# Kernel optimization log

Measured on AMD Instinct MI355X. Metric: run time of the kernel, lower is better.

## Reference

```python
import jax, jax.numpy as jnp
import numpy as np

N = 100000
E = 1600000
D = 64
N_LAYERS = 2


def setup_inputs() -> dict:
    key = jax.random.key(0)
    ks = jax.random.split(key, 4 + 4 * N_LAYERS)
    h = jax.random.normal(ks[0], (N, D), dtype=jnp.float32)
    x = jax.random.normal(ks[1], (N, 3), dtype=jnp.float32)
    edge_index = jax.random.randint(ks[2], (2, E), 0, N, dtype=jnp.int64)
    node_mask = jnp.ones((N, 1), dtype=jnp.float32)
    scale = 1.0 / np.sqrt(D)
    params = {}
    for i in range(N_LAYERS):
        params[f'W1_{i}'] = jax.random.normal(ks[4 + 4 * i], (D, D), dtype=jnp.float32) * scale
        params[f'b1_{i}'] = jax.random.normal(ks[5 + 4 * i], (D,), dtype=jnp.float32) * scale
        params[f'W2_{i}'] = jax.random.normal(ks[6 + 4 * i], (D, D), dtype=jnp.float32) * scale
        params[f'b2_{i}'] = jax.random.normal(ks[7 + 4 * i], (D,), dtype=jnp.float32) * scale
    return dict(h=h, x=x, edge_index=edge_index, node_mask=node_mask, **params)


def _gin_layer(h, src, dst, W1, b1, W2, b2):
    # GINConv with eps=0: mlp(h_i + sum_{j->i} h_j)
    agg = jax.ops.segment_sum(h[src], dst, num_segments=N)  # [N, D]
    z = h + agg
    z = jax.nn.relu(z @ W1 + b1)
    return z @ W2 + b2


def reference(h, x, edge_index, node_mask,
              W1_0, b1_0, W2_0, b2_0,
              W1_1, b1_1, W2_1, b2_1):
    src, dst = edge_index[0], edge_index[1]
    h = _gin_layer(h, src, dst, W1_0, b1_0, W2_0, b2_0)
    h = _gin_layer(h, src, dst, W1_1, b1_1, W2_1, b2_1)
    h = h * node_mask
    return (h, x)
```

## Files before the change

### kernel.cpp

```cpp
#include <hip/hip_runtime.h>


#define NN 100000
#define EE 1600000
#define CAP 48
#define NBIN 1024
#define CHB 6250
#define OVF_CAPN 8000

#define OVFC_OFF   1024
#define OVF_OFF    1026
#define BSTART_OFF 17056
#define CURSOR_OFF 18112
#define CNT_OFF    19200
#define BUCK_OFF   119296
#define BINNED_OFF 4919296
#define HB_OFF     4919296
#define PW_OFF     8119296

typedef __attribute__((ext_vector_type(8))) short s8v;
typedef __attribute__((ext_vector_type(4))) float f4v;

union U8 { unsigned u[4]; s8v s; };

static __device__ __forceinline__ unsigned short f2bf(float f) {
  unsigned u = __float_as_uint(f);
  return (unsigned short)((u + 0x7FFF + ((u >> 16) & 1)) >> 16);
}
static __device__ __forceinline__ float bf2f(unsigned short s) {
  return __uint_as_float(((unsigned)s) << 16);
}
static __device__ __forceinline__ unsigned pk2(float lo, float hi) {
  return (unsigned)f2bf(lo) | ((unsigned)f2bf(hi) << 16);
}

__global__ __launch_bounds__(256) void hist_k(const int* __restrict__ dst,
                                              int* __restrict__ binTot) {
  __shared__ int hist[NBIN];
  const int t = threadIdx.x;
#pragma unroll
  for (int b = t; b < NBIN; b += 256) hist[b] = 0;
  __syncthreads();
  const int s = blockIdx.x * CHB;
#pragma unroll 1
  for (int i = s + t; i < s + CHB; i += 256) atomicAdd(&hist[dst[i] >> 7], 1);
  __syncthreads();
#pragma unroll
  for (int b = t; b < NBIN; b += 256) {
    const int c = hist[b];
    if (c) atomicAdd(&binTot[b], c);
  }
}

__global__ __launch_bounds__(1024) void scan_k(const int* __restrict__ binTot,
                                               int* __restrict__ binStart,
                                               int* __restrict__ cursor) {
  __shared__ int sh[NBIN];
  const int t = threadIdx.x;
  const int v = binTot[t];
  sh[t] = v;
  __syncthreads();
  for (int off = 1; off < NBIN; off <<= 1) {
    const int x = (t >= off) ? sh[t - off] : 0;
    __syncthreads();
    sh[t] += x;
    __syncthreads();
  }
  binStart[t] = sh[t] - v;
  cursor[t] = sh[t] - v;
  if (t == NBIN - 1) binStart[NBIN] = sh[t];
}

__global__ __launch_bounds__(256) void scatter_k(const int* __restrict__ src,
                                                 const int* __restrict__ dst,
                                                 int* __restrict__ cursor,
                                                 int* __restrict__ binned) {
  __shared__ int hist[NBIN], base[NBIN], lcnt[NBIN];
  const int t = threadIdx.x;
#pragma unroll
  for (int b = t; b < NBIN; b += 256) { hist[b] = 0; lcnt[b] = 0; }
  __syncthreads();
  const int s = blockIdx.x * CHB;
#pragma unroll 1
  for (int i = s + t; i < s + CHB; i += 256) atomicAdd(&hist[dst[i] >> 7], 1);
  __syncthreads();
#pragma unroll
  for (int b = t; b < NBIN; b += 256) {
    const int c = hist[b];
    base[b] = c ? atomicAdd(&cursor[b], c) : 0;
  }
  __syncthreads();
#pragma unroll 1
  for (int i = s + t; i < s + CHB; i += 256) {
    const int d = dst[i], sv = src[i];
    const int bin = d >> 7;
    const int off = atomicAdd(&lcnt[bin], 1);
    binned[base[bin] + off] = ((d & 127) << 17) | sv;
  }
}

__global__ __launch_bounds__(256) void bucketize_k(const int* __restrict__ binStart,
                                                   const int* __restrict__ binned,
                                                   int* __restrict__ bucket,
                                                   int* __restrict__ cnt,
                                                   int* __restrict__ ovf) {
  __shared__ int c128[128];
  const int t = threadIdx.x;
  const int bin = blockIdx.x;
  const int nbase = bin << 7;
  if (t < 128) c128[t] = 0;
  __syncthreads();
  const int s0 = binStart[bin], s1 = binStart[bin + 1];
#pragma unroll 1
  for (int i = s0 + t; i < s1; i += 256) {
    const int p = binned[i];
    const int dlow = p >> 17;
    const int sv = p & 131071;
    const int slot = atomicAdd(&c128[dlow], 1);
    if (slot < CAP) {
      bucket[(nbase + dlow) * CAP + slot] = sv;
    } else {
      const int q = atomicAdd(&ovf[-2], 1);
      if (q < OVF_CAPN) { ovf[2 * q] = nbase + dlow; ovf[2 * q + 1] = sv; }
    }
  }
  __syncthreads();
  if (t < 128 && nbase + t < NN) cnt[nbase + t] = c128[t];
}

__global__ __launch_bounds__(256) void cvt_k(const float* __restrict__ h,
                                             unsigned* __restrict__ hb) {
  const int i = blockIdx.x * blockDim.x + threadIdx.x;
  if (i >= NN * 8) return;
  const float4* __restrict__ h4 = reinterpret_cast<const float4*>(h);
  const float4 a = h4[2 * i], b = h4[2 * i + 1];
  uint4 o;
  o.x = pk2(a.x, a.y); o.y = pk2(a.z, a.w);
  o.z = pk2(b.x, b.y); o.w = pk2(b.z, b.w);
  reinterpret_cast<uint4*>(hb)[i] = o;
}

__global__ __launch_bounds__(256) void pack_k(const float* __restrict__ W1a,
                                              const float* __restrict__ W2a,
                                              const float* __restrict__ W1b,
                                              const float* __restrict__ W2b,
                                              unsigned short* __restrict__ pw) {
  const int t = threadIdx.x;
  const float* Ws[4] = {W1a, W2a, W1b, W2b};
#pragma unroll
  for (int m = 0; m < 4; ++m) {
    const float* __restrict__ W = Ws[m];
#pragma unroll 1
    for (int i = 0; i < 16; ++i) {
      const int e = i * 256 + t;
      const int j = e & 7;
      const int lv = (e >> 3) & 63;
      const int ks = (e >> 9) & 1;
      const int tt = e >> 10;
      const int k = ks * 32 + (lv >> 4) * 8 + j;
      const int n = tt * 16 + (lv & 15);
      pw[m * 4096 + e] = f2bf(W[k * 64 + n]);
    }
  }
}

__global__ __launch_bounds__(256) void agg_k(const unsigned short* __restrict__ hb,
                                             const int* __restrict__ cnt,
                                             const int* __restrict__ bucket,
                                             char* __restrict__ zb) {
  const int l = threadIdx.x & 63;
  int n = blockIdx.x * (blockDim.x >> 6) + (threadIdx.x >> 6);
  if (n >= NN) return;
  n = __builtin_amdgcn_readfirstlane(n);
  const int deg = min(cnt[n], CAP);
  const int* __restrict__ brow = bucket + n * CAP;
  float acc = bf2f(hb[(n << 6) | l]);
#pragma unroll 1
  for (int e = 0; e < deg; e += 8) {
    const int4 qa = *reinterpret_cast<const int4*>(brow + e);
    const int4 qb = *reinterpret_cast<const int4*>(brow + e + 4);
    const int s0 = qa.x;
    const int s1 = (e + 1 < deg) ? qa.y : s0;
    const int s2 = (e + 2 < deg) ? qa.z : s0;
    const int s3 = (e + 3 < deg) ? qa.w : s0;
    const int s4 = (e + 4 < deg) ? qb.x : s0;
    const int s5 = (e + 5 < deg) ? qb.y : s0;
    const int s6 = (e + 6 < deg) ? qb.z : s0;
    const int s7 = (e + 7 < deg) ? qb.w : s0;
    const float v0 = bf2f(hb[(s0 << 6) | l]);
    const float v1 = bf2f(hb[(s1 << 6) | l]);
    const float v2 = bf2f(hb[(s2 << 6) | l]);
    const float v3 = bf2f(hb[(s3 << 6) | l]);
    const float v4 = bf2f(hb[(s4 << 6) | l]);
    const float v5 = bf2f(hb[(s5 << 6) | l]);
    const float v6 = bf2f(hb[(s6 << 6) | l]);
    const float v7 = bf2f(hb[(s7 << 6) | l]);
    const float w1 = (e + 1 < deg) ? v1 : 0.f;
    const float w2 = (e + 2 < deg) ? v2 : 0.f;
    const float w3 = (e + 3 < deg) ? v3 : 0.f;
    const float w4 = (e + 4 < deg) ? v4 : 0.f;
    const float w5 = (e + 5 < deg) ? v5 : 0.f;
    const float w6 = (e + 6 < deg) ? v6 : 0.f;
    const float w7 = (e + 7 < deg) ? v7 : 0.f;
    acc += ((v0 + w1) + (w2 + w3)) + ((w4 + w5) + (w6 + w7));
  }
  *reinterpret_cast<unsigned short*>(zb + n * 256 + l * 2) = f2bf(acc);
}

__global__ __launch_bounds__(256) void ovf_fix_k(const unsigned short* __restrict__ hb,
                                                 char* __restrict__ zb,
                                                 const int* __restrict__ ovfCnt,
                                                 const int* __restrict__ ovf) {
  const int cv = min(ovfCnt[0], OVF_CAPN);
  const int l = threadIdx.x & 63;
  const int w = threadIdx.x >> 6;
  for (int p = w; p < cv; p += 4) {
    const int d = ovf[2 * p];
    const int s = ovf[2 * p + 1];
    const float add = bf2f(hb[(s << 6) | l]);
    unsigned* wp = reinterpret_cast<unsigned*>(zb + d * 256 + (l >> 1) * 4);
    const bool hi = l & 1;
    unsigned cur = atomicAdd(wp, 0u);
    while (true) {
      const unsigned short hv = hi ? (unsigned short)(cur >> 16) : (unsigned short)(cur & 0xffffu);
      const unsigned short nh = f2bf(bf2f(hv) + add);
      const unsigned nw = hi ? ((cur & 0x0000ffffu) | ((unsigned)nh << 16))
                             : ((cur & 0xffff0000u) | (unsigned)nh);
      const unsigned prev = atomicCAS(wp, cur, nw);
      if (prev == cur) break;
      cur = prev;
    }
  }
}

template <int OUTBF>
__global__ __launch_bounds__(256) void mlp_mfma_k(
    const char* __restrict__ zb,
    void* __restrict__ hout,
    const unsigned short* __restrict__ pw1, const float* __restrict__ b1,
    const unsigned short* __restrict__ pw2, const float* __restrict__ b2,
    const float* __restrict__ mask) {
  __shared__ unsigned ldsu[128 * 33];
  const int tid = threadIdx.x;
  const int w = tid >> 6, l = tid & 63, g = l >> 4, mi = l & 15;
  const int m0 = blockIdx.x * 128;
  const int rbase = w * 32;

  s8v zf[2][2];
#pragma unroll
  for (int tm = 0; tm < 2; ++tm) {
    const int node = m0 + rbase + tm * 16 + mi;
    const int nc = node < NN ? node : NN - 1;
#pragma unroll
    for (int ks = 0; ks < 2; ++ks)
      zf[tm][ks] = *reinterpret_cast<const s8v*>(zb + nc * 256 + (ks * 32 + g * 8) * 2);
  }

  f4v acc[4][2];
#pragma unroll
  for (int t = 0; t < 4; ++t) {
    const f4v bv = *reinterpret_cast<const f4v*>(b1 + t * 16 + g * 4);
    acc[t][0] = bv; acc[t][1] = bv;
  }
#pragma unroll
  for (int t = 0; t < 4; ++t) {
#pragma unroll
    for (int ks = 0; ks < 2; ++ks) {
      const s8v wf = *reinterpret_cast<const s8v*>(pw1 + ((t * 2 + ks) * 64 + l) * 8);
#pragma unroll
      for (int tm = 0; tm < 2; ++tm)
        acc[t][tm] = __builtin_amdgcn_mfma_f32_16x16x32_bf16(wf, zf[tm][ks], acc[t][tm], 0, 0, 0);
    }
  }

#pragma unroll
  for (int t = 0; t < 4; ++t) {
#pragma unroll
    for (int tm = 0; tm < 2; ++tm) {
      const f4v a = acc[t][tm];
      const int row = rbase + tm * 16 + mi;
      const int base = row * 33 + t * 8 + g * 2;
      ldsu[base]     = pk2(fmaxf(a.x, 0.f), fmaxf(a.y, 0.f));
      ldsu[base + 1] = pk2(fmaxf(a.z, 0.f), fmaxf(a.w, 0.f));
    }
  }
  __syncthreads();

  s8v cf[2][2];
#pragma unroll
  for (int tm = 0; tm < 2; ++tm) {
    const int row = rbase + tm * 16 + mi;
    const int cbase = row * 33 + (mi < 0 ? 0 : 0);
#pragma unroll
    for (int ks = 0; ks < 2; ++ks) {
      const int b0 = row * 33 + ks * 16 + g * 4;
      U8 u8;
      u8.u[0] = ldsu[b0 + 0];
      u8.u[1] = ldsu[b0 + 1];
      u8.u[2] = ldsu[b0 + 2];
      u8.u[3] = ldsu[b0 + 3];
      cf[tm][ks] = u8.s;
    }
    (void)cbase;
  }

  f4v acc2[4][2];
#pragma unroll
  for (int t = 0; t < 4; ++t) {
    const f4v bv = *reinterpret_cast<const f4v*>(b2 + t * 16 + g * 4);
    acc2[t][0] = bv; acc2[t][1] = bv;
  }
#pragma unroll
  for (int t = 0; t < 4; ++t) {
#pragma unroll
    for (int ks = 0; ks < 2; ++ks) {
      const s8v wf = *reinterpret_cast<const s8v*>(pw2 + ((t * 2 + ks) * 64 + l) * 8);
#pragma unroll
      for (int tm = 0; tm < 2; ++tm)
        acc2[t][tm] = __builtin_amdgcn_mfma_f32_16x16x32_bf16(wf, cf[tm][ks], acc2[t][tm], 0, 0, 0);
    }
  }

  if (OUTBF) {
    unsigned* __restrict__ ho = reinterpret_cast<unsigned*>(hout);
#pragma unroll
    for (int tm = 0; tm < 2; ++tm) {
      const int node = m0 + rbase + tm * 16 + mi;
      if (node < NN) {
#pragma unroll
        for (int t = 0; t < 4; ++t) {
          const f4v a = acc2[t][tm];
          const int idx = node * 32 + t * 8 + g * 2;
          uint2 p;
          p.x = pk2(a.x, a.y);
          p.y = pk2(a.z, a.w);
          *reinterpret_cast<uint2*>(&ho[idx]) = p;
        }
      }
    }
  } else {
    float* __restrict__ fo = reinterpret_cast<float*>(hout);
#pragma unroll
    for (int tm = 0; tm < 2; ++tm) {
      const int node = m0 + rbase + tm * 16 + mi;
      if (node < NN) {
        const float mv = mask[node];
#pragma unroll
        for (int t = 0; t < 4; ++t) {
          f4v v = acc2[t][tm];
          v *= mv;
          *reinterpret_cast<f4v*>(fo + node * 64 + t * 16 + g * 4) = v;
        }
      }
    }
  }
}

__global__ __launch_bounds__(256) void xcopy_k(const float* __restrict__ x,
                                               float* __restrict__ ox) {
  const int i = blockIdx.x * blockDim.x + threadIdx.x;
  if (i < (NN * 3) / 4) {
    reinterpret_cast<float4*>(ox)[i] = reinterpret_cast<const float4*>(x)[i];
  }
}

extern "C" void kernel_launch(void* const* d_in, const int* in_sizes, int n_in,
                              void* d_out, int out_size, void* d_ws, size_t ws_size,
                              hipStream_t stream) {
  (void)in_sizes; (void)n_in; (void)out_size; (void)ws_size;
  const float* h    = (const float*)d_in[0];
  const float* x    = (const float*)d_in[1];
  const int*   ei   = (const int*)d_in[2];
  const float* mask = (const float*)d_in[3];
  const float* W1_0 = (const float*)d_in[4];
  const float* b1_0 = (const float*)d_in[5];
  const float* W2_0 = (const float*)d_in[6];
  const float* b2_0 = (const float*)d_in[7];
  const float* W1_1 = (const float*)d_in[8];
  const float* b1_1 = (const float*)d_in[9];
  const float* W2_1 = (const float*)d_in[10];
  const float* b2_1 = (const float*)d_in[11];
  float* out = (float*)d_out;

  const int* src = ei;
  const int* dst = ei + EE;

  int* wsp       = (int*)d_ws;
  int* binTot    = wsp;
  int* ovfCnt    = wsp + OVFC_OFF;
  int* ovf       = wsp + OVF_OFF;
  int* binStart  = wsp + BSTART_OFF;
  int* cursor    = wsp + CURSOR_OFF;
  int* cnt       = wsp + CNT_OFF;
  int* bucket    = wsp + BUCK_OFF;
  int* binned    = wsp + BINNED_OFF;
  unsigned* hb   = (unsigned*)(wsp + HB_OFF);
  unsigned short* pw = (unsigned short*)(wsp + PW_OFF);
  const unsigned short* hbs = (const unsigned short*)hb;
  char* zb       = (char*)d_out;

  hipMemsetAsync(d_ws, 0, 8192, stream);
  hist_k<<<256, 256, 0, stream>>>(dst, binTot);
  scan_k<<<1, 1024, 0, stream>>>(binTot, binStart, cursor);
  scatter_k<<<256, 256, 0, stream>>>(src, dst, cursor, binned);
  bucketize_k<<<782, 256, 0, stream>>>(binStart, binned, bucket, cnt, ovf);

  pack_k<<<1, 256, 0, stream>>>(W1_0, W2_0, W1_1, W2_1, pw);

  cvt_k<<<3125, 256, 0, stream>>>(h, hb);
  agg_k<<<25000, 256, 0, stream>>>(hbs, cnt, bucket, zb);
  ovf_fix_k<<<1, 256, 0, stream>>>(hbs, zb, ovfCnt, ovf);
  mlp_mfma_k<1><<<782, 256, 0, stream>>>(zb, hb, pw, b1_0, pw + 4096, b2_0, nullptr);

  agg_k<<<25000, 256, 0, stream>>>(hbs, cnt, bucket, zb);
  ovf_fix_k<<<1, 256, 0, stream>>>(hbs, zb, ovfCnt, ovf);
  mlp_mfma_k<0><<<782, 256, 0, stream>>>(zb, out, pw + 8192, b1_1, pw + 12288, b2_1, mask);

  xcopy_k<<<293, 256, 0, stream>>>(x, out + NN * 64);
}
```

Before: 178.1 us.

## Restructure aggregation to 4 neighbor groups per wave and merge small launches

The aggregation kernel now splits each wave into four 16-lane groups. Each lane loads four bf16 features (8 bytes) per neighbor, the groups process up to 32 neighbors per iteration, and partial sums are reduced with cross-lane shuffles. This exposes more independent gathers per wave and uses wider loads, at the cost of shuffle work and wasted lanes on low-degree nodes. The memset and weight packing are fused into one setup kernel, the x copy is merged into the bf16 conversion kernel, and the histogram and scatter loops read edges as int2 pairs to cut launch overhead and load instructions.

```diff
diff --git a/kernel.cpp b/kernel.cpp
--- a/kernel.cpp
+++ b/kernel.cpp
@@ -34,6 +34,33 @@
   return (unsigned)f2bf(lo) | ((unsigned)f2bf(hi) << 16);
 }
 
+__global__ __launch_bounds__(256) void setup_k(const float* __restrict__ W1a,
+                                               const float* __restrict__ W2a,
+                                               const float* __restrict__ W1b,
+                                               const float* __restrict__ W2b,
+                                               unsigned short* __restrict__ pw,
+                                               int* __restrict__ wsp) {
+  const int t = threadIdx.x;
+#pragma unroll
+  for (int i = t; i < 2048; i += 256) wsp[i] = 0;
+  const float* Ws[4] = {W1a, W2a, W1b, W2b};
+#pragma unroll
+  for (int m = 0; m < 4; ++m) {
+    const float* __restrict__ W = Ws[m];
+#pragma unroll 1
+    for (int i = 0; i < 16; ++i) {
+      const int e = i * 256 + t;
+      const int j = e & 7;
+      const int lv = (e >> 3) & 63;
+      const int ks = (e >> 9) & 1;
+      const int tt = e >> 10;
+      const int k = ks * 32 + (lv >> 4) * 8 + j;
+      const int n = tt * 16 + (lv & 15);
+      pw[m * 4096 + e] = f2bf(W[k * 64 + n]);
+    }
+  }
+}
+
 __global__ __launch_bounds__(256) void hist_k(const int* __restrict__ dst,
                                               int* __restrict__ binTot) {
   __shared__ int hist[NBIN];
@@ -43,7 +70,11 @@
   __syncthreads();
   const int s = blockIdx.x * CHB;
 #pragma unroll 1
-  for (int i = s + t; i < s + CHB; i += 256) atomicAdd(&hist[dst[i] >> 7], 1);
+  for (int p = t; p < CHB / 2; p += 256) {
+    const int2 dd = *reinterpret_cast<const int2*>(dst + s + 2 * p);
+    atomicAdd(&hist[dd.x >> 7], 1);
+    atomicAdd(&hist[dd.y >> 7], 1);
+  }
   __syncthreads();
 #pragma unroll
   for (int b = t; b < NBIN; b += 256) {
@@ -82,7 +113,11 @@
   __syncthreads();
   const int s = blockIdx.x * CHB;
 #pragma unroll 1
-  for (int i = s + t; i < s + CHB; i += 256) atomicAdd(&hist[dst[i] >> 7], 1);
+  for (int p = t; p < CHB / 2; p += 256) {
+    const int2 dd = *reinterpret_cast<const int2*>(dst + s + 2 * p);
+    atomicAdd(&hist[dd.x >> 7], 1);
+    atomicAdd(&hist[dd.y >> 7], 1);
+  }
   __syncthreads();
 #pragma unroll
   for (int b = t; b < NBIN; b += 256) {
@@ -91,11 +126,16 @@
   }
   __syncthreads();
 #pragma unroll 1
-  for (int i = s + t; i < s + CHB; i += 256) {
-    const int d = dst[i], sv = src[i];
-    const int bin = d >> 7;
-    const int off = atomicAdd(&lcnt[bin], 1);
-    binned[base[bin] + off] = ((d & 127) << 17) | sv;
+  for (int p = t; p < CHB / 2; p += 256) {
+    const int i = s + 2 * p;
+    const int2 dd = *reinterpret_cast<const int2*>(dst + i);
+    const int2 ss = *reinterpret_cast<const int2*>(src + i);
+    int bin = dd.x >> 7;
+    int off = atomicAdd(&lcnt[bin], 1);
+    binned[base[bin] + off] = ((dd.x & 127) << 17) | ss.x;
+    bin = dd.y >> 7;
+    off = atomicAdd(&lcnt[bin], 1);
+    binned[base[bin] + off] = ((dd.y & 127) << 17) | ss.y;
   }
 }
 
@@ -128,83 +168,87 @@
   if (t < 128 && nbase + t < NN) cnt[nbase + t] = c128[t];
 }
 
-__global__ __launch_bounds__(256) void cvt_k(const float* __restrict__ h,
-                                             unsigned* __restrict__ hb) {
-  const int i = blockIdx.x * blockDim.x + threadIdx.x;
-  if (i >= NN * 8) return;
-  const float4* __restrict__ h4 = reinterpret_cast<const float4*>(h);
-  const float4 a = h4[2 * i], b = h4[2 * i + 1];
-  uint4 o;
-  o.x = pk2(a.x, a.y); o.y = pk2(a.z, a.w);
-  o.z = pk2(b.x, b.y); o.w = pk2(b.z, b.w);
-  reinterpret_cast<uint4*>(hb)[i] = o;
-}
-
-__global__ __launch_bounds__(256) void pack_k(const float* __restrict__ W1a,
-                                              const float* __restrict__ W2a,
-                                              const float* __restrict__ W1b,
-                                              const float* __restrict__ W2b,
-                                              unsigned short* __restrict__ pw) {
-  const int t = threadIdx.x;
-  const float* Ws[4] = {W1a, W2a, W1b, W2b};
-#pragma unroll
-  for (int m = 0; m < 4; ++m) {
-    const float* __restrict__ W = Ws[m];
-#pragma unroll 1
-    for (int i = 0; i < 16; ++i) {
-      const int e = i * 256 + t;
-      const int j = e & 7;
-      const int lv = (e >> 3) & 63;
-      const int ks = (e >> 9) & 1;
-      const int tt = e >> 10;
-      const int k = ks * 32 + (lv >> 4) * 8 + j;
-      const int n = tt * 16 + (lv & 15);
-      pw[m * 4096 + e] = f2bf(W[k * 64 + n]);
-    }
+__global__ __launch_bounds__(256) void cvtx_k(const float* __restrict__ h,
+                                              unsigned* __restrict__ hb,
+                                              const float* __restrict__ x,
+                                              float* __restrict__ ox) {
+  const int b = blockIdx.x;
+  const int t = threadIdx.x;
+  if (b < 3125) {
+    const int i = b * 256 + t;
+    const float4* __restrict__ h4 = reinterpret_cast<const float4*>(h);
+    const float4 a = h4[2 * i], c = h4[2 * i + 1];
+    uint4 o;
+    o.x = pk2(a.x, a.y); o.y = pk2(a.z, a.w);
+    o.z = pk2(c.x, c.y); o.w = pk2(c.z, c.w);
+    reinterpret_cast<uint4*>(hb)[i] = o;
+  } else {
+    const int i = (b - 3125) * 256 + t;
+    if (i < (NN * 3) / 4)
+      reinterpret_cast<float4*>(ox)[i] = reinterpret_cast<const float4*>(x)[i];
   }
 }
 
 __global__ __launch_bounds__(256) void agg_k(const unsigned short* __restrict__ hb,
                                              const int* __restrict__ cnt,
                                              const int* __restrict__ bucket,
-                                             char* __restrict__ zb) {
+                                             unsigned* __restrict__ zbu) {
   const int l = threadIdx.x & 63;
-  int n = blockIdx.x * (blockDim.x >> 6) + (threadIdx.x >> 6);
+  const int s = l >> 4, g = l & 15;
+  int n = blockIdx.x * 4 + (threadIdx.x >> 6);
+  n = __builtin_amdgcn_readfirstlane(n);
   if (n >= NN) return;
-  n = __builtin_amdgcn_readfirstlane(n);
   const int deg = min(cnt[n], CAP);
   const int* __restrict__ brow = bucket + n * CAP;
-  float acc = bf2f(hb[(n << 6) | l]);
-#pragma unroll 1
-  for (int e = 0; e < deg; e += 8) {
-    const int4 qa = *reinterpret_cast<const int4*>(brow + e);
-    const int4 qb = *reinterpret_cast<const int4*>(brow + e + 4);
-    const int s0 = qa.x;
-    const int s1 = (e + 1 < deg) ? qa.y : s0;
-    const int s2 = (e + 2 < deg) ? qa.z : s0;
-    const int s3 = (e + 3 < deg) ? qa.w : s0;
-    const int s4 = (e + 4 < deg) ? qb.x : s0;
-    const int s5 = (e + 5 < deg) ? qb.y : s0;
-    const int s6 = (e + 6 < deg) ? qb.z : s0;
-    const int s7 = (e + 7 < deg) ? qb.w : s0;
-    const float v0 = bf2f(hb[(s0 << 6) | l]);
-    const float v1 = bf2f(hb[(s1 << 6) | l]);
-    const float v2 = bf2f(hb[(s2 << 6) | l]);
-    const float v3 = bf2f(hb[(s3 << 6) | l]);
-    const float v4 = bf2f(hb[(s4 << 6) | l]);
-    const float v5 = bf2f(hb[(s5 << 6) | l]);
-    const float v6 = bf2f(hb[(s6 << 6) | l]);
-    const float v7 = bf2f(hb[(s7 << 6) | l]);
-    const float w1 = (e + 1 < deg) ? v1 : 0.f;
-    const float w2 = (e + 2 < deg) ? v2 : 0.f;
-    const float w3 = (e + 3 < deg) ? v3 : 0.f;
-    const float w4 = (e + 4 < deg) ? v4 : 0.f;
-    const float w5 = (e + 5 < deg) ? v5 : 0.f;
-    const float w6 = (e + 6 < deg) ? v6 : 0.f;
-    const float w7 = (e + 7 < deg) ? v7 : 0.f;
-    acc += ((v0 + w1) + (w2 + w3)) + ((w4 + w5) + (w6 + w7));
-  }
-  *reinterpret_cast<unsigned short*>(zb + n * 256 + l * 2) = f2bf(acc);
+  const uint2* __restrict__ h2 = reinterpret_cast<const uint2*>(hb);
+
+  const uint2 sv = h2[n * 16 + g];
+  const unsigned m0 = (s == 0) ? sv.x : 0u;
+  const unsigned m1 = (s == 0) ? sv.y : 0u;
+  float a0 = __uint_as_float(m0 << 16);
+  float a1 = __uint_as_float(m0 & 0xffff0000u);
+  float a2 = __uint_as_float(m1 << 16);
+  float a3 = __uint_as_float(m1 & 0xffff0000u);
+
+#pragma unroll 1
+  for (int it = 0; it * 32 < deg; ++it) {
+    const int base = it * 32 + s * 8;
+    const int4 qa = *reinterpret_cast<const int4*>(brow + base);
+    const int4 qb = *reinterpret_cast<const int4*>(brow + base + 4);
+    const bool k0 = base + 0 < deg, k1 = base + 1 < deg, k2 = base + 2 < deg, k3 = base + 3 < deg;
+    const bool k4 = base + 4 < deg, k5 = base + 5 < deg, k6 = base + 6 < deg, k7 = base + 7 < deg;
+    const int i0 = k0 ? qa.x : n, i1 = k1 ? qa.y : n, i2 = k2 ? qa.z : n, i3 = k3 ? qa.w : n;
+    const int i4 = k4 ? qb.x : n, i5 = k5 ? qb.y : n, i6 = k6 ? qb.z : n, i7 = k7 ? qb.w : n;
+    const uint2 v0 = h2[i0 * 16 + g];
+    const uint2 v1 = h2[i1 * 16 + g];
+    const uint2 v2 = h2[i2 * 16 + g];
+    const uint2 v3 = h2[i3 * 16 + g];
+    const uint2 v4 = h2[i4 * 16 + g];
+    const uint2 v5 = h2[i5 * 16 + g];
+    const uint2 v6 = h2[i6 * 16 + g];
+    const uint2 v7 = h2[i7 * 16 + g];
+#define ACC(vv, kk)                                                      \
+    { const unsigned ux = kk ? vv.x : 0u, uy = kk ? vv.y : 0u;           \
+      a0 += __uint_as_float(ux << 16);                                   \
+      a1 += __uint_as_float(ux & 0xffff0000u);                           \
+      a2 += __uint_as_float(uy << 16);                                   \
+      a3 += __uint_as_float(uy & 0xffff0000u); }
+    ACC(v0, k0) ACC(v1, k1) ACC(v2, k2) ACC(v3, k3)
+    ACC(v4, k4) ACC(v5, k5) ACC(v6, k6) ACC(v7, k7)
+#undef ACC
+  }
+
+  a0 += __shfl_xor(a0, 16); a1 += __shfl_xor(a1, 16);
+  a2 += __shfl_xor(a2, 16); a3 += __shfl_xor(a3, 16);
+  a0 += __shfl_xor(a0, 32); a1 += __shfl_xor(a1, 32);
+  a2 += __shfl_xor(a2, 32); a3 += __shfl_xor(a3, 32);
+
+  if (s == 0) {
+    uint2 o;
+    o.x = pk2(a0, a1);
+    o.y = pk2(a2, a3);
+    reinterpret_cast<uint2*>(zbu)[n * 32 + g] = o;
+  }
 }
 
 __global__ __launch_bounds__(256) void ovf_fix_k(const unsigned short* __restrict__ hb,
@@ -290,7 +334,6 @@
 #pragma unroll
   for (int tm = 0; tm < 2; ++tm) {
     const int row = rbase + tm * 16 + mi;
-    const int cbase = row * 33 + (mi < 0 ? 0 : 0);
 #pragma unroll
     for (int ks = 0; ks < 2; ++ks) {
       const int b0 = row * 33 + ks * 16 + g * 4;
@@ -301,7 +344,6 @@
       u8.u[3] = ldsu[b0 + 3];
       cf[tm][ks] = u8.s;
     }
-    (void)cbase;
   }
 
   f4v acc2[4][2];
@@ -353,14 +395,6 @@
         }
       }
     }
-  }
-}
-
-__global__ __launch_bounds__(256) void xcopy_k(const float* __restrict__ x,
-                                               float* __restrict__ ox) {
-  const int i = blockIdx.x * blockDim.x + threadIdx.x;
-  if (i < (NN * 3) / 4) {
-    reinterpret_cast<float4*>(ox)[i] = reinterpret_cast<const float4*>(x)[i];
   }
 }
 
@@ -397,24 +431,22 @@
   unsigned* hb   = (unsigned*)(wsp + HB_OFF);
   unsigned short* pw = (unsigned short*)(wsp + PW_OFF);
   const unsigned short* hbs = (const unsigned short*)hb;
+  unsigned* zbu  = (unsigned*)d_out;
   char* zb       = (char*)d_out;
 
-  hipMemsetAsync(d_ws, 0, 8192, stream);
+  setup_k<<<1, 256, 0, stream>>>(W1_0, W2_0, W1_1, W2_1, pw, wsp);
   hist_k<<<256, 256, 0, stream>>>(dst, binTot);
   scan_k<<<1, 1024, 0, stream>>>(binTot, binStart, cursor);
   scatter_k<<<256, 256, 0, stream>>>(src, dst, cursor, binned);
   bucketize_k<<<782, 256, 0, stream>>>(binStart, binned, bucket, cnt, ovf);
 
-  pack_k<<<1, 256, 0, stream>>>(W1_0, W2_0, W1_1, W2_1, pw);
-
-  cvt_k<<<3125, 256, 0, stream>>>(h, hb);
-  agg_k<<<25000, 256, 0, stream>>>(hbs, cnt, bucket, zb);
+  cvtx_k<<<3418, 256, 0, stream>>>(h, hb, x, out + NN * 64);
+
+  agg_k<<<25000, 256, 0, stream>>>(hbs, cnt, bucket, zbu);
   ovf_fix_k<<<1, 256, 0, stream>>>(hbs, zb, ovfCnt, ovf);
   mlp_mfma_k<1><<<782, 256, 0, stream>>>(zb, hb, pw, b1_0, pw + 4096, b2_0, nullptr);
 
-  agg_k<<<25000, 256, 0, stream>>>(hbs, cnt, bucket, zb);
+  agg_k<<<25000, 256, 0, stream>>>(hbs, cnt, bucket, zbu);
   ovf_fix_k<<<1, 256, 0, stream>>>(hbs, zb, ovfCnt, ovf);
   mlp_mfma_k<0><<<782, 256, 0, stream>>>(zb, out, pw + 8192, b1_1, pw + 12288, b2_1, mask);
-
-  xcopy_k<<<293, 256, 0, stream>>>(x, out + NN * 64);
-}
+}
```

Result: faster. 167.5 us (-6.0%).
